# Optimization experiments

Measured on AMD Instinct MI355X. Metric: run time of the kernel, lower is better.

## Reference

```python
import jax, jax.numpy as jnp
import numpy as np

D_MODEL = 1024
N_HEADS = 16
D_K = D_MODEL // N_HEADS


def setup_inputs() -> dict:
    key = jax.random.key(0)
    ks = jax.random.split(key, 12)
    B, S = 2, 2048
    scale = 1.0 / np.sqrt(D_MODEL)
    inp = {
        "query": jax.random.normal(ks[0], (B, S, D_MODEL), jnp.float32),
        "key": jax.random.normal(ks[1], (B, S, D_MODEL), jnp.float32),
        "value": jax.random.normal(ks[2], (B, S, D_MODEL), jnp.float32),
        "weights": jax.random.uniform(ks[3], (B, S), jnp.float32),
        "wq": jax.random.normal(ks[4], (D_MODEL, D_MODEL), jnp.float32) * scale,
        "bq": jnp.zeros((D_MODEL,), jnp.float32),
        "wk": jax.random.normal(ks[5], (D_MODEL, D_MODEL), jnp.float32) * scale,
        "bk": jnp.zeros((D_MODEL,), jnp.float32),
        "wv": jax.random.normal(ks[6], (D_MODEL, D_MODEL), jnp.float32) * scale,
        "bv": jnp.zeros((D_MODEL,), jnp.float32),
        "wo": jax.random.normal(ks[7], (D_MODEL, D_MODEL), jnp.float32) * scale,
        "bo": jnp.zeros((D_MODEL,), jnp.float32),
    }
    return inp


def _split_heads(x):
    # (B, S, d_model) -> (B, H, S, d_k)
    B, S, _ = x.shape
    return x.reshape(B, S, N_HEADS, D_K).transpose(0, 2, 1, 3)


def reference(query, key, value, weights, wq, bq, wk, bk, wv, bv, wo, bo):
    Q = _split_heads(query @ wq + bq)
    K = _split_heads(key @ wk + bk)
    V = _split_heads(value @ wv + bv)
    # scores: (B, H, n_q, n_kv)
    scores = jnp.einsum("bhqd,bhkd->bhqk", Q, K) / np.sqrt(D_K)
    log_w = jnp.log(weights + 1e-20)[:, None, None, :]  # (B,1,1,n_kv)
    attn = jax.nn.softmax(scores + log_w, axis=-1)
    out = jnp.einsum("bhqk,bhkd->bhqd", attn, V)
    B, H, S, Dk = out.shape
    out = out.transpose(0, 2, 1, 3).reshape(B, S, D_MODEL)
    return out @ wo + bo
```

## Files before the change

### kernel.cpp

```cpp
#include <hip/hip_runtime.h>

typedef unsigned short u16;
typedef __bf16 bf16x8 __attribute__((ext_vector_type(8)));
typedef float f32x4 __attribute__((ext_vector_type(4)));
typedef float f32x16 __attribute__((ext_vector_type(16)));

#define D_MODEL 1024
#define NH 16
#define DKD 64
#define BB 2
#define SS 2048
#define QSCL 0.18033688011112042f

#if __has_builtin(__builtin_amdgcn_exp2f)
#define EXP2(x) __builtin_amdgcn_exp2f(x)
#else
#define EXP2(x) exp2f(x)
#endif

__device__ __forceinline__ u16 f2bf(float f) {
  union { float f; unsigned u; } x; x.f = f;
  unsigned r = x.u + 0x7fffu + ((x.u >> 16) & 1u);
  return (u16)(r >> 16);
}

__device__ __forceinline__ void gld16(const u16* g, u16* l) {
  __builtin_amdgcn_global_load_lds((__attribute__((address_space(1))) void*)(g),
                                   (__attribute__((address_space(3))) void*)(l),
                                   16, 0, 0);
}

extern "C" __global__ void __launch_bounds__(256) kprep_conv(
    const float* __restrict__ q, const float* __restrict__ k, const float* __restrict__ v,
    const float* __restrict__ wts,
    u16* __restrict__ xq, u16* __restrict__ xk, u16* __restrict__ xv,
    float* __restrict__ lw)
{
  int z = blockIdx.y;
  if (blockIdx.x == 4096) {
    if (z == 0) {
      int i = threadIdx.x * 16;
      #pragma unroll
      for (int j = 0; j < 16; j += 4) {
        float4 val = *(const float4*)(wts + i + j);
        lw[i + j + 0] = log2f(val.x + 1e-20f) - 16.0f;
        lw[i + j + 1] = log2f(val.y + 1e-20f) - 16.0f;
        lw[i + j + 2] = log2f(val.z + 1e-20f) - 16.0f;
        lw[i + j + 3] = log2f(val.w + 1e-20f) - 16.0f;
      }
    }
    return;
  }
  const float* s = z == 0 ? q : (z == 1 ? k : v);
  u16* d = z == 0 ? xq : (z == 1 ? xk : xv);
  int i = (blockIdx.x * 256 + threadIdx.x) * 4;
  float4 val = *(const float4*)(s + i);
  ushort4 o;
  o.x = f2bf(val.x); o.y = f2bf(val.y); o.z = f2bf(val.z); o.w = f2bf(val.w);
  *(ushort4*)(d + i) = o;
}

extern "C" __global__ void __launch_bounds__(256) kprep_wt(
    const float* __restrict__ w0, const float* __restrict__ w1,
    const float* __restrict__ w2, const float* __restrict__ w3,
    u16* __restrict__ o0, u16* __restrict__ o1, u16* __restrict__ o2, u16* __restrict__ o3)
{
  const float* src; u16* dst;
  switch (blockIdx.z) {
    case 0: src = w0; dst = o0; break;
    case 1: src = w1; dst = o1; break;
    case 2: src = w2; dst = o2; break;
    default: src = w3; dst = o3; break;
  }
  __shared__ float t[32][33];
  int n0 = blockIdx.x * 32, k0 = blockIdx.y * 32;
  int tx = threadIdx.x & 31, ty = threadIdx.x >> 5;
  #pragma unroll
  for (int i = 0; i < 32; i += 8)
    t[ty + i][tx] = src[(k0 + ty + i) * D_MODEL + n0 + tx];
  __syncthreads();
  #pragma unroll
  for (int i = 0; i < 32; i += 8)
    dst[(size_t)(n0 + ty + i) * D_MODEL + k0 + tx] = f2bf(t[tx][ty + i]);
}

extern "C" __global__ void __launch_bounds__(256) ktrans_v(
    const u16* __restrict__ src, u16* __restrict__ dst)
{
  __shared__ u16 T[64][72];
  int bh = blockIdx.y; int s0 = blockIdx.x * 64;
  int tid = threadIdx.x;
  int r = tid >> 3, c = (tid & 7) * 8;
  #pragma unroll
  for (int i = 0; i < 2; ++i)
    *(bf16x8*)&T[r + i * 32][c] = *(const bf16x8*)&src[((size_t)bh * SS + s0 + r + i * 32) * DKD + c];
  __syncthreads();
  #pragma unroll
  for (int i = 0; i < 2; ++i) {
    int dk = r + i * 32;
    ushort4 o0, o1;
    o0.x = T[c + 0][dk]; o0.y = T[c + 1][dk]; o0.z = T[c + 2][dk]; o0.w = T[c + 3][dk];
    o1.x = T[c + 4][dk]; o1.y = T[c + 5][dk]; o1.z = T[c + 6][dk]; o1.w = T[c + 7][dk];
    *(ushort4*)&dst[((size_t)bh * DKD + dk) * SS + s0 + c] = o0;
    *(ushort4*)&dst[((size_t)bh * DKD + dk) * SS + s0 + c + 4] = o1;
  }
}

__device__ __forceinline__ void gemm_tile(const u16* __restrict__ Ag, const u16* __restrict__ Bg,
                                          u16* As, u16* Bs, f32x4 acc[4][4], int tid)
{
  int lane = tid & 63;
  int lr = lane & 15, lg = lane >> 4;
  int w = tid >> 6, wr = w >> 1, wc = w & 1;
  for (int k0 = 0; k0 < D_MODEL; k0 += 32) {
    #pragma unroll
    for (int c = 0; c < 2; ++c) {
      int idx = tid + c * 256;
      int row = idx >> 2, col = (idx & 3) * 8;
      gld16(Ag + row * D_MODEL + k0 + col, As + idx * 8);
      gld16(Bg + row * D_MODEL + k0 + col, Bs + idx * 8);
    }
    __syncthreads();
    bf16x8 af[4], bfr[4];
    #pragma unroll
    for (int mi = 0; mi < 4; ++mi)
      af[mi] = *(const bf16x8*)(As + (wr * 64 + mi * 16 + lr) * 32 + lg * 8);
    #pragma unroll
    for (int nj = 0; nj < 4; ++nj)
      bfr[nj] = *(const bf16x8*)(Bs + (wc * 64 + nj * 16 + lr) * 32 + lg * 8);
    #pragma unroll
    for (int mi = 0; mi < 4; ++mi)
      #pragma unroll
      for (int nj = 0; nj < 4; ++nj)
        acc[mi][nj] = __builtin_amdgcn_mfma_f32_16x16x32_bf16(af[mi], bfr[nj], acc[mi][nj], 0, 0, 0);
    __syncthreads();
  }
}

extern "C" __global__ void __launch_bounds__(256) kgemm_qkv(
    const u16* __restrict__ xq, const u16* __restrict__ xk, const u16* __restrict__ xv,
    const u16* __restrict__ wqt, const u16* __restrict__ wkt, const u16* __restrict__ wvt,
    const float* __restrict__ bq, const float* __restrict__ bk, const float* __restrict__ bv,
    u16* __restrict__ Qb, u16* __restrict__ Kb, u16* __restrict__ Vb)
{
  __shared__ u16 As[128 * 32], Bs[128 * 32];
  int z = blockIdx.z;
  const u16* X  = z == 0 ? xq : (z == 1 ? xk : xv);
  const u16* Wt = z == 0 ? wqt : (z == 1 ? wkt : wvt);
  const float* bias = z == 0 ? bq : (z == 1 ? bk : bv);
  u16* dst = z == 0 ? Qb : (z == 1 ? Kb : Vb);
  int tid = threadIdx.x;
  f32x4 zero = {0.f, 0.f, 0.f, 0.f};
  f32x4 acc[4][4];
  #pragma unroll
  for (int i = 0; i < 4; ++i)
    #pragma unroll
    for (int j = 0; j < 4; ++j) acc[i][j] = zero;
  int m0 = blockIdx.y * 128, n0 = blockIdx.x * 128;
  gemm_tile(X + (size_t)m0 * D_MODEL, Wt + (size_t)n0 * D_MODEL, As, Bs, acc, tid);
  int lane = tid & 63, lr = lane & 15, lg = lane >> 4;
  int w = tid >> 6, wr = w >> 1, wc = w & 1;
  float scl = (z == 0) ? QSCL : 1.0f;
  #pragma unroll
  for (int mi = 0; mi < 4; ++mi)
    #pragma unroll
    for (int nj = 0; nj < 4; ++nj) {
      int n = n0 + wc * 64 + nj * 16 + lr;
      float bs = bias[n];
      int h = n >> 6, dk = n & 63;
      #pragma unroll
      for (int j = 0; j < 4; ++j) {
        int m = m0 + wr * 64 + mi * 16 + lg * 4 + j;
        int b = m >> 11, s = m & 2047;
        dst[(((size_t)(b * NH + h)) * SS + s) * DKD + dk] = f2bf((acc[mi][nj][j] + bs) * scl);
      }
    }
}

extern "C" __global__ void __launch_bounds__(256) kgemm_o(
    const u16* __restrict__ AO, const u16* __restrict__ wot,
    const float* __restrict__ bo, float* __restrict__ out)
{
  __shared__ u16 As[128 * 32], Bs[128 * 32];
  int tid = threadIdx.x;
  f32x4 zero = {0.f, 0.f, 0.f, 0.f};
  f32x4 acc[4][4];
  #pragma unroll
  for (int i = 0; i < 4; ++i)
    #pragma unroll
    for (int j = 0; j < 4; ++j) acc[i][j] = zero;
  int m0 = blockIdx.y * 128, n0 = blockIdx.x * 128;
  gemm_tile(AO + (size_t)m0 * D_MODEL, wot + (size_t)n0 * D_MODEL, As, Bs, acc, tid);
  int lane = tid & 63, lr = lane & 15, lg = lane >> 4;
  int w = tid >> 6, wr = w >> 1, wc = w & 1;
  #pragma unroll
  for (int mi = 0; mi < 4; ++mi)
    #pragma unroll
    for (int nj = 0; nj < 4; ++nj) {
      int n = n0 + wc * 64 + nj * 16 + lr;
      float bs = bo[n];
      #pragma unroll
      for (int j = 0; j < 4; ++j) {
        int m = m0 + wr * 64 + mi * 16 + lg * 4 + j;
        out[(size_t)m * D_MODEL + n] = acc[mi][nj][j] + bs;
      }
    }
}

extern "C" __global__ void __launch_bounds__(512, 4) kattn(
    const u16* __restrict__ Qb, const u16* __restrict__ Kb, const u16* __restrict__ Vt,
    const float* __restrict__ lw2, u16* __restrict__ AO)
{
  __shared__ __align__(16) char smem[4 * 16384 + 8192];
  float* lwf = (float*)(smem + 65536);

  int tid = threadIdx.x, lane = tid & 63, w = tid >> 6;
  int lq = lane & 31, hi = lane >> 5;
  int qw = w & 3, par = w >> 2;

  int n = blockIdx.x;
  int xcd = n & 7, slot = n >> 3;
  int bh = xcd + 8 * (slot >> 4);
  int q0 = (slot & 15) * 128;
  int b = bh >> 4, h = bh & 15;

  const u16* Qg = Qb + ((size_t)bh * SS + q0 + qw * 32) * DKD;
  const u16* Kg = Kb + (size_t)bh * SS * DKD;
  const u16* Vg = Vt + (size_t)bh * DKD * SS;
  const float* lwb = lw2 + b * SS;

  *(float4*)&lwf[tid * 4] = *(const float4*)(lwb + tid * 4);

  bf16x8 qf[4];
  #pragma unroll
  for (int kc = 0; kc < 4; ++kc)
    qf[kc] = *(const bf16x8*)(Qg + lq * DKD + kc * 16 + hi * 8);

  f32x16 acco[2] = {};
  float lsp[4] = {0.f, 0.f, 0.f, 0.f};

  int srow = tid >> 3, sc = ((tid & 7) ^ (srow & 7)) * 8;

#define KSLOT(sl) ((u16*)(smem + (sl) * 16384))
#define VSLOT(sl) ((u16*)(smem + (sl) * 16384 + 8192))
#define STAGE(t, sl) do { \
    gld16(Kg + (size_t)((t) * 64 + srow) * DKD + sc, KSLOT(sl) + tid * 8); \
    gld16(Vg + (size_t)srow * SS + (t) * 64 + sc, VSLOT(sl) + tid * 8); \
  } while (0)

  STAGE(0, 0); STAGE(1, 1); STAGE(2, 2); STAGE(3, 3);
  for (int i = 0; i < 16; ++i) {
    if (i < 15) asm volatile("s_waitcnt vmcnt(4) lgkmcnt(0)" ::: "memory");
    else        asm volatile("s_waitcnt vmcnt(0) lgkmcnt(0)" ::: "memory");
    __builtin_amdgcn_s_barrier();
    __builtin_amdgcn_sched_barrier(0);

    int t = 2 * i + par;
    int bi = t & 3;
    int kv0 = t * 64;
    const u16* Kp = KSLOT(bi);
    const u16* Vp = VSLOT(bi);

    f32x16 st[2];
    #pragma unroll
    for (int nh = 0; nh < 2; ++nh)
      #pragma unroll
      for (int g = 0; g < 4; ++g) {
        f32x4 lv = *(const f32x4*)&lwf[kv0 + nh * 32 + 4 * hi + 8 * g];
        st[nh][4 * g + 0] = lv[0]; st[nh][4 * g + 1] = lv[1];
        st[nh][4 * g + 2] = lv[2]; st[nh][4 * g + 3] = lv[3];
      }

    __builtin_amdgcn_s_setprio(1);
    #pragma unroll
    for (int kc = 0; kc < 4; ++kc) {
      bf16x8 kf0 = *(const bf16x8*)&Kp[(lq) * 64      + (((kc * 2 + hi) ^ (lq & 7)) * 8)];
      bf16x8 kf1 = *(const bf16x8*)&Kp[(32 + lq) * 64 + (((kc * 2 + hi) ^ (lq & 7)) * 8)];
      st[0] = __builtin_amdgcn_mfma_f32_32x32x16_bf16(kf0, qf[kc], st[0], 0, 0, 0);
      st[1] = __builtin_amdgcn_mfma_f32_32x32x16_bf16(kf1, qf[kc], st[1], 0, 0, 0);
    }
    __builtin_amdgcn_s_setprio(0);

    unsigned wd[2][8];
    #pragma unroll
    for (int nh = 0; nh < 2; ++nh)
      #pragma unroll
      for (int r2 = 0; r2 < 8; ++r2) {
        float plo = EXP2(st[nh][2 * r2]);
        float phi = EXP2(st[nh][2 * r2 + 1]);
        lsp[r2 & 3] += plo + phi;
        union { unsigned u; __bf16 b2[2]; } cv;
        cv.b2[0] = (__bf16)plo; cv.b2[1] = (__bf16)phi;
        wd[nh][r2] = cv.u;
      }

    bf16x8 Pb[4];
    #pragma unroll
    for (int c = 0; c < 4; ++c) {
      int nh = c >> 1, j0 = 4 * (c & 1);
      auto s1 = __builtin_amdgcn_permlane32_swap(wd[nh][j0 + 0], wd[nh][j0 + 2], false, false);
      auto s2 = __builtin_amdgcn_permlane32_swap(wd[nh][j0 + 1], wd[nh][j0 + 3], false, false);
      union { unsigned u[4]; bf16x8 v; } pb;
      pb.u[0] = s1[0]; pb.u[1] = s2[0]; pb.u[2] = s1[1]; pb.u[3] = s2[1];
      Pb[c] = pb.v;
    }

    __builtin_amdgcn_s_setprio(1);
    #pragma unroll
    for (int c = 0; c < 4; ++c) {
      bf16x8 vf0 = *(const bf16x8*)&Vp[(lq) * 64      + (((c * 2 + hi) ^ (lq & 7)) * 8)];
      bf16x8 vf1 = *(const bf16x8*)&Vp[(32 + lq) * 64 + (((c * 2 + hi) ^ (lq & 7)) * 8)];
      acco[0] = __builtin_amdgcn_mfma_f32_32x32x16_bf16(vf0, Pb[c], acco[0], 0, 0, 0);
      acco[1] = __builtin_amdgcn_mfma_f32_32x32x16_bf16(vf1, Pb[c], acco[1], 0, 0, 0);
    }
    __builtin_amdgcn_s_setprio(0);

    __builtin_amdgcn_sched_barrier(0);
    __builtin_amdgcn_s_barrier();
    int tn = 2 * i + 4;
    if (tn < 32) { STAGE(tn, tn & 3); STAGE(tn + 1, (tn + 1) & 3); }
  }
#undef STAGE

  float lsum_part = (lsp[0] + lsp[1]) + (lsp[2] + lsp[3]);
  float* comb = (float*)smem;
  int coff = (qw * 64 + lane) * 34;
  if (par == 1) {
    #pragma unroll
    for (int d = 0; d < 2; ++d)
      #pragma unroll
      for (int g = 0; g < 8; ++g)
        *(float2*)&comb[coff + (d * 8 + g) * 2] = make_float2(acco[d][2 * g], acco[d][2 * g + 1]);
    comb[coff + 32] = lsum_part;
  }
  __syncthreads();
  if (par == 0) {
    #pragma unroll
    for (int d = 0; d < 2; ++d)
      #pragma unroll
      for (int g = 0; g < 8; ++g) {
        float2 v = *(const float2*)&comb[coff + (d * 8 + g) * 2];
        acco[d][2 * g] += v.x; acco[d][2 * g + 1] += v.y;
      }
    lsum_part += comb[coff + 32];
    float lsum = lsum_part + __shfl_xor(lsum_part, 32);
    float inv = 1.0f / lsum;
    int s = q0 + qw * 32 + lq;
    size_t base = ((size_t)b * SS + s) * D_MODEL + h * DKD;
    #pragma unroll
    for (int dh = 0; dh < 2; ++dh)
      #pragma unroll
      for (int g = 0; g < 4; ++g) {
        ushort4 o;
        o.x = f2bf(acco[dh][4 * g + 0] * inv);
        o.y = f2bf(acco[dh][4 * g + 1] * inv);
        o.z = f2bf(acco[dh][4 * g + 2] * inv);
        o.w = f2bf(acco[dh][4 * g + 3] * inv);
        *(ushort4*)(AO + base + dh * 32 + 4 * hi + 8 * g) = o;
      }
  }
#undef KSLOT
#undef VSLOT
}

extern "C" void kernel_launch(void* const* d_in, const int* in_sizes, int n_in,
                              void* d_out, int out_size, void* d_ws, size_t ws_size,
                              hipStream_t stream) {
  const float* query = (const float*)d_in[0];
  const float* key_  = (const float*)d_in[1];
  const float* value = (const float*)d_in[2];
  const float* wts   = (const float*)d_in[3];
  const float* wq = (const float*)d_in[4];
  const float* bq = (const float*)d_in[5];
  const float* wk = (const float*)d_in[6];
  const float* bk = (const float*)d_in[7];
  const float* wv = (const float*)d_in[8];
  const float* bv = (const float*)d_in[9];
  const float* wo = (const float*)d_in[10];
  const float* bo = (const float*)d_in[11];
  float* out = (float*)d_out;

  char* ws = (char*)d_ws;
  const size_t MB = 1024 * 1024;
  u16* Xq  = (u16*)(ws + 0 * MB);
  u16* Xk  = (u16*)(ws + 8 * MB);
  u16* Xv  = (u16*)(ws + 16 * MB);
  u16* WqT = (u16*)(ws + 24 * MB);
  u16* WkT = (u16*)(ws + 26 * MB);
  u16* WvT = (u16*)(ws + 28 * MB);
  u16* WoT = (u16*)(ws + 30 * MB);
  u16* Qb  = (u16*)(ws + 32 * MB);
  u16* Kb  = (u16*)(ws + 40 * MB);
  u16* Vb  = (u16*)(ws + 48 * MB);
  u16* AO  = (u16*)(ws + 56 * MB);
  float* lwbuf = (float*)(ws + 64 * MB);
  u16* VtT = (u16*)(ws + 16 * MB);

  kprep_conv<<<dim3(4097, 3), 256, 0, stream>>>(query, key_, value, wts, Xq, Xk, Xv, lwbuf);
  kprep_wt<<<dim3(32, 32, 4), 256, 0, stream>>>(wq, wk, wv, wo, WqT, WkT, WvT, WoT);
  kgemm_qkv<<<dim3(8, 32, 3), 256, 0, stream>>>(Xq, Xk, Xv, WqT, WkT, WvT, bq, bk, bv, Qb, Kb, Vb);
  ktrans_v<<<dim3(32, 32), 256, 0, stream>>>(Vb, VtT);
  kattn<<<512, 512, 0, stream>>>(Qb, Kb, VtT, lwbuf, AO);
  kgemm_o<<<dim3(8, 32), 256, 0, stream>>>(AO, WoT, bo, out);
}
```

Measured before the change: 134.9 us.

## Widen GEMM K-tile to 64 with XOR-swizzled LDS and smaller O-proj M-tile

The shared GEMM tile loop now stages 64-wide K slices instead of 32, halving the number of barrier pairs per tile. It applies an XOR swizzle on the 16-byte column chunks to avoid LDS bank conflicts on the fragment reads. The output projection gets its own loop with a 64x128 tile, doubling its grid to 512 blocks for better CU occupancy on a small GEMM. The cost is more LDS per block and more per-block overhead in the O-projection.

```diff
diff --git a/kernel.cpp b/kernel.cpp
--- a/kernel.cpp
+++ b/kernel.cpp
@@ -112,27 +112,32 @@
   int lane = tid & 63;
   int lr = lane & 15, lg = lane >> 4;
   int w = tid >> 6, wr = w >> 1, wc = w & 1;
-  for (int k0 = 0; k0 < D_MODEL; k0 += 32) {
-    #pragma unroll
-    for (int c = 0; c < 2; ++c) {
+  int sr7 = lr & 7;
+  for (int k0 = 0; k0 < D_MODEL; k0 += 64) {
+    #pragma unroll
+    for (int c = 0; c < 4; ++c) {
       int idx = tid + c * 256;
-      int row = idx >> 2, col = (idx & 3) * 8;
+      int row = idx >> 3, c3 = idx & 7;
+      int col = (c3 ^ (row & 7)) * 8;
       gld16(Ag + row * D_MODEL + k0 + col, As + idx * 8);
       gld16(Bg + row * D_MODEL + k0 + col, Bs + idx * 8);
     }
     __syncthreads();
-    bf16x8 af[4], bfr[4];
-    #pragma unroll
-    for (int mi = 0; mi < 4; ++mi)
-      af[mi] = *(const bf16x8*)(As + (wr * 64 + mi * 16 + lr) * 32 + lg * 8);
-    #pragma unroll
-    for (int nj = 0; nj < 4; ++nj)
-      bfr[nj] = *(const bf16x8*)(Bs + (wc * 64 + nj * 16 + lr) * 32 + lg * 8);
-    #pragma unroll
-    for (int mi = 0; mi < 4; ++mi)
+    #pragma unroll
+    for (int kk = 0; kk < 2; ++kk) {
+      bf16x8 af[4], bfr[4];
+      #pragma unroll
+      for (int mi = 0; mi < 4; ++mi)
+        af[mi] = *(const bf16x8*)(As + (wr * 64 + mi * 16 + lr) * 64 + (((kk * 4 + lg) ^ sr7) * 8));
       #pragma unroll
       for (int nj = 0; nj < 4; ++nj)
-        acc[mi][nj] = __builtin_amdgcn_mfma_f32_16x16x32_bf16(af[mi], bfr[nj], acc[mi][nj], 0, 0, 0);
+        bfr[nj] = *(const bf16x8*)(Bs + (wc * 64 + nj * 16 + lr) * 64 + (((kk * 4 + lg) ^ sr7) * 8));
+      #pragma unroll
+      for (int mi = 0; mi < 4; ++mi)
+        #pragma unroll
+        for (int nj = 0; nj < 4; ++nj)
+          acc[mi][nj] = __builtin_amdgcn_mfma_f32_16x16x32_bf16(af[mi], bfr[nj], acc[mi][nj], 0, 0, 0);
+    }
     __syncthreads();
   }
 }
@@ -143,7 +148,7 @@
     const float* __restrict__ bq, const float* __restrict__ bk, const float* __restrict__ bv,
     u16* __restrict__ Qb, u16* __restrict__ Kb, u16* __restrict__ Vb)
 {
-  __shared__ u16 As[128 * 32], Bs[128 * 32];
+  __shared__ u16 As[128 * 64], Bs[128 * 64];
   int z = blockIdx.z;
   const u16* X  = z == 0 ? xq : (z == 1 ? xk : xv);
   const u16* Wt = z == 0 ? wqt : (z == 1 ? wkt : wvt);
@@ -181,27 +186,64 @@
     const u16* __restrict__ AO, const u16* __restrict__ wot,
     const float* __restrict__ bo, float* __restrict__ out)
 {
-  __shared__ u16 As[128 * 32], Bs[128 * 32];
+  __shared__ u16 As[64 * 64], Bs[128 * 64];
   int tid = threadIdx.x;
+  int lane = tid & 63, lr = lane & 15, lg = lane >> 4;
+  int w = tid >> 6, wr = w & 1, wc = w >> 1;
+  int sr7 = lr & 7;
+  int m0 = blockIdx.y * 64, n0 = blockIdx.x * 128;
+  const u16* Ag = AO + (size_t)m0 * D_MODEL;
+  const u16* Bg = wot + (size_t)n0 * D_MODEL;
   f32x4 zero = {0.f, 0.f, 0.f, 0.f};
-  f32x4 acc[4][4];
-  #pragma unroll
-  for (int i = 0; i < 4; ++i)
+  f32x4 acc[2][4];
+  #pragma unroll
+  for (int i = 0; i < 2; ++i)
     #pragma unroll
     for (int j = 0; j < 4; ++j) acc[i][j] = zero;
-  int m0 = blockIdx.y * 128, n0 = blockIdx.x * 128;
-  gemm_tile(AO + (size_t)m0 * D_MODEL, wot + (size_t)n0 * D_MODEL, As, Bs, acc, tid);
-  int lane = tid & 63, lr = lane & 15, lg = lane >> 4;
-  int w = tid >> 6, wr = w >> 1, wc = w & 1;
-  #pragma unroll
-  for (int mi = 0; mi < 4; ++mi)
+
+  for (int k0 = 0; k0 < D_MODEL; k0 += 64) {
+    #pragma unroll
+    for (int c = 0; c < 2; ++c) {
+      int idx = tid + c * 256;
+      int row = idx >> 3, c3 = idx & 7;
+      int col = (c3 ^ (row & 7)) * 8;
+      gld16(Ag + row * D_MODEL + k0 + col, As + idx * 8);
+    }
+    #pragma unroll
+    for (int c = 0; c < 4; ++c) {
+      int idx = tid + c * 256;
+      int row = idx >> 3, c3 = idx & 7;
+      int col = (c3 ^ (row & 7)) * 8;
+      gld16(Bg + row * D_MODEL + k0 + col, Bs + idx * 8);
+    }
+    __syncthreads();
+    #pragma unroll
+    for (int kk = 0; kk < 2; ++kk) {
+      bf16x8 af[2], bfr[4];
+      #pragma unroll
+      for (int mi = 0; mi < 2; ++mi)
+        af[mi] = *(const bf16x8*)(As + (wr * 32 + mi * 16 + lr) * 64 + (((kk * 4 + lg) ^ sr7) * 8));
+      #pragma unroll
+      for (int nj = 0; nj < 4; ++nj)
+        bfr[nj] = *(const bf16x8*)(Bs + (wc * 64 + nj * 16 + lr) * 64 + (((kk * 4 + lg) ^ sr7) * 8));
+      #pragma unroll
+      for (int mi = 0; mi < 2; ++mi)
+        #pragma unroll
+        for (int nj = 0; nj < 4; ++nj)
+          acc[mi][nj] = __builtin_amdgcn_mfma_f32_16x16x32_bf16(af[mi], bfr[nj], acc[mi][nj], 0, 0, 0);
+    }
+    __syncthreads();
+  }
+
+  #pragma unroll
+  for (int mi = 0; mi < 2; ++mi)
     #pragma unroll
     for (int nj = 0; nj < 4; ++nj) {
       int n = n0 + wc * 64 + nj * 16 + lr;
       float bs = bo[n];
       #pragma unroll
       for (int j = 0; j < 4; ++j) {
-        int m = m0 + wr * 64 + mi * 16 + lg * 4 + j;
+        int m = m0 + wr * 32 + mi * 16 + lg * 4 + j;
         out[(size_t)m * D_MODEL + n] = acc[mi][nj][j] + bs;
       }
     }
@@ -401,5 +443,5 @@
   kgemm_qkv<<<dim3(8, 32, 3), 256, 0, stream>>>(Xq, Xk, Xv, WqT, WkT, WvT, bq, bk, bv, Qb, Kb, Vb);
   ktrans_v<<<dim3(32, 32), 256, 0, stream>>>(Vb, VtT);
   kattn<<<512, 512, 0, stream>>>(Qb, Kb, VtT, lwbuf, AO);
-  kgemm_o<<<dim3(8, 32), 256, 0, stream>>>(AO, WoT, bo, out);
-}
+  kgemm_o<<<dim3(8, 64), 256, 0, stream>>>(AO, WoT, bo, out);
+}
```

New measurement: 136.8 us. No clear change (+1.4%).
